# Optimization experiments

Hardware: AMD Instinct MI355X
Metric: run time of the kernel (lower is better)

Reference implementation:

```python
import jax, jax.numpy as jnp
import numpy as np

B, T, H, E = 4, 8192, 512, 2048  # batch, seq, hidden (num_dims), embed (num_embeds)
LN_EPS = 1e-5


def _layernorm(x, g, b):
    m = x.mean(-1, keepdims=True)
    v = ((x - m) ** 2).mean(-1, keepdims=True)
    return (x - m) * jax.lax.rsqrt(v + LN_EPS) * g + b


def setup_inputs() -> dict:
    key = jax.random.key(0)
    ks = jax.random.split(key, 8)
    C = 64
    tri = jnp.tril(jnp.ones((C, C), jnp.float32))
    kw = 1.0 / np.sqrt(C)
    inp = {
        "x": jax.random.normal(ks[0], (B, T, H), jnp.float32),
        "ln1_g": jnp.ones((H,), jnp.float32),
        "ln1_b": jnp.zeros((H,), jnp.float32),
        # TriLinear weights: (features, features), lower-triangular masked at init
        "W1": jax.random.uniform(ks[1], (C, C), jnp.float32, -kw, kw) * tri,
        "W2": jax.random.uniform(ks[2], (C, C), jnp.float32, -kw, kw) * tri,
        "ln2_g": jnp.ones((H,), jnp.float32),
        "ln2_b": jnp.zeros((H,), jnp.float32),
        # ffw: Linear(H->E), sin, Linear(E->H); stored (in, out)
        "fw1": jax.random.uniform(ks[3], (H, E), jnp.float32, -1.0 / np.sqrt(H), 1.0 / np.sqrt(H)),
        "fb1": jax.random.uniform(ks[4], (E,), jnp.float32, -1.0 / np.sqrt(H), 1.0 / np.sqrt(H)),
        "fw2": jax.random.uniform(ks[5], (E, H), jnp.float32, -1.0 / np.sqrt(E), 1.0 / np.sqrt(E)),
        "fb2": jax.random.uniform(ks[6], (H,), jnp.float32, -1.0 / np.sqrt(E), 1.0 / np.sqrt(E)),
        "chunk_size": 64,
        "stride": 32,
    }
    return inp


def reference(x, ln1_g, ln1_b, W1, W2, ln2_g, ln2_b, fw1, fb1, fw2, fb2, chunk_size, stride):
    Bb, Tt, Hh = x.shape
    C = chunk_size
    starts = jnp.arange(0, Tt, stride)              # (N,)
    pos = starts[:, None] + jnp.arange(C)           # (N, C)
    valid = (pos < Tt)
    vmask = valid[None, :, :, None].astype(x.dtype)
    safe = jnp.minimum(pos, Tt - 1)
    chunks = x[:, safe] * vmask                     # (B, N, C, H): padded chunks (zeros past T)
    resid = chunks
    cn = _layernorm(chunks, ln1_g, ln1_b)
    tri = jnp.tril(jnp.ones((C, C), x.dtype))
    # TriLinear on time axis (torch transposes to (B,H,C); einsum avoids the transpose)
    y = jnp.einsum('ts,bnsh->bnth', W1 * tri, cn)
    y = jnp.einsum('ts,bnsh->bnth', W2 * tri, y)
    c2 = y + resid
    h = _layernorm(c2, ln2_g, ln2_b)
    h = jnp.sin(h @ fw1 + fb1) @ fw2 + fb2
    out_chunks = (h + c2) * vmask                   # zero the padded tail (torch truncates it)
    flat = safe.reshape(-1)                         # (N*C,)
    out = jnp.zeros_like(x).at[:, flat].add(out_chunks.reshape(Bb, -1, Hh))
    counts = jnp.zeros((Tt,), x.dtype).at[flat].add(valid.reshape(-1).astype(x.dtype))
    return out / jnp.maximum(counts, 1.0)[None, :, None]
```

## Files before the change

### kernel.cpp

```cpp
#include <hip/hip_runtime.h>
#include <math.h>

#define TB 4
#define TT 8192
#define TH 512
#define TE 2048
#define NCHUNK 256
#define GCTOT 1024

typedef unsigned short u16;
typedef short bf8v __attribute__((ext_vector_type(8)));
typedef float f4v __attribute__((ext_vector_type(4)));

__device__ __forceinline__ float bu2f(u16 u) {
    unsigned int x = ((unsigned int)u) << 16; float f; __builtin_memcpy(&f, &x, 4); return f;
}
__device__ __forceinline__ u16 f2bu(float f) {
    unsigned int x; __builtin_memcpy(&x, &f, 4);
    x = x + 0x7fffu + ((x >> 16) & 1u);
    return (u16)(x >> 16);
}

__global__ __launch_bounds__(256) void make_Mt(const float* __restrict__ W1,
                                               const float* __restrict__ W2,
                                               float* __restrict__ Mt) {
    __shared__ float w1[64 * 64];
    __shared__ float w2[64 * 64];
    for (int i = threadIdx.x; i < 4096; i += 256) { w1[i] = W1[i]; w2[i] = W2[i]; }
    __syncthreads();
    for (int i = threadIdx.x; i < 4096; i += 256) {
        int t = i >> 6, s = i & 63;
        float a = 0.f;
        if (t >= s) for (int k = s; k <= t; ++k) a += w2[t * 64 + k] * w1[k * 64 + s];
        Mt[s * 64 + t] = a;
    }
}

__global__ __launch_bounds__(256) void transpose_b(const float* __restrict__ in,
                                                   u16* __restrict__ out, int R, int C) {
    __shared__ u16 tile[64][65];
    const int bx = blockIdx.x, by = blockIdx.y;
    const int tx = threadIdx.x & 63, ty = threadIdx.x >> 6;
#pragma unroll
    for (int i = 0; i < 16; ++i) {
        int r = ty + i * 4;
        tile[r][tx] = f2bu(in[(size_t)(by * 64 + r) * C + bx * 64 + tx]);
    }
    __syncthreads();
#pragma unroll
    for (int i = 0; i < 16; ++i) {
        int r = ty + i * 4;
        out[(size_t)(bx * 64 + r) * R + by * 64 + tx] = tile[tx][r];
    }
}

__global__ __launch_bounds__(256) void ln_stats(const float* __restrict__ x,
                                                float2* __restrict__ st) {
    const int wave = threadIdx.x >> 6, lane = threadIdx.x & 63;
    const size_t row = (size_t)blockIdx.x * 4 + wave;
    const float4* p = (const float4*)(x + row * TH);
    float4 a = p[lane * 2], b = p[lane * 2 + 1];
    float s = 0.f, q = 0.f;
    float v[8] = {a.x, a.y, a.z, a.w, b.x, b.y, b.z, b.w};
#pragma unroll
    for (int i = 0; i < 8; ++i) { s += v[i]; q += v[i] * v[i]; }
#pragma unroll
    for (int o = 32; o; o >>= 1) { s += __shfl_xor(s, o); q += __shfl_xor(q, o); }
    const float mean = s * (1.f / TH);
    float var = q * (1.f / TH) - mean * mean;
    if (var < 0.f) var = 0.f;
    if (lane == 0) st[row] = make_float2(mean, rsqrtf(var + 1e-5f));
}

__global__ __launch_bounds__(256) void ln_rows(const u16* __restrict__ in,
                                               u16* __restrict__ out,
                                               const float* __restrict__ g,
                                               const float* __restrict__ b) {
    const int wave = threadIdx.x >> 6, lane = threadIdx.x & 63;
    const size_t row = (size_t)blockIdx.x * 4 + wave;
    uint4 raw = *((const uint4*)(in + row * TH) + lane);
    const u16* e = (const u16*)&raw;
    float v[8]; float s = 0.f, q = 0.f;
#pragma unroll
    for (int i = 0; i < 8; ++i) { v[i] = bu2f(e[i]); s += v[i]; q += v[i] * v[i]; }
#pragma unroll
    for (int o = 32; o; o >>= 1) { s += __shfl_xor(s, o); q += __shfl_xor(q, o); }
    const float mean = s * (1.f / TH);
    float var = q * (1.f / TH) - mean * mean;
    if (var < 0.f) var = 0.f;
    const float rstd = rsqrtf(var + 1e-5f);
    float4 g0 = ((const float4*)g)[lane * 2], g1 = ((const float4*)g)[lane * 2 + 1];
    float4 b0 = ((const float4*)b)[lane * 2], b1 = ((const float4*)b)[lane * 2 + 1];
    float ge[8] = {g0.x, g0.y, g0.z, g0.w, g1.x, g1.y, g1.z, g1.w};
    float be[8] = {b0.x, b0.y, b0.z, b0.w, b1.x, b1.y, b1.z, b1.w};
    u16 ov[8];
#pragma unroll
    for (int i = 0; i < 8; ++i) ov[i] = f2bu((v[i] - mean) * rstd * ge[i] + be[i]);
    *((uint4*)(out + row * TH) + lane) = *(uint4*)ov;
}

__global__ __launch_bounds__(256) void trilinear_f(const float* __restrict__ x,
                                                   const float2* __restrict__ st,
                                                   const float* __restrict__ g,
                                                   const float* __restrict__ bb,
                                                   const float* __restrict__ Mt,
                                                   u16* __restrict__ c2s,
                                                   int gc0) {
    const int ln = blockIdx.x;
    const int gc = gc0 + ln;
    const int b = gc >> 8, n = gc & 255;
    const int h = (blockIdx.y << 8) + threadIdx.x;
    const int base = n * 32;
    const float gh = g[h], bh = bb[h];
    float acc[64];
#pragma unroll
    for (int t = 0; t < 64; ++t) acc[t] = 0.f;
    for (int s = 0; s < 64; ++s) {
        int pos = base + s; if (pos > TT - 1) pos = TT - 1;
        const size_t ro = (size_t)b * TT + pos;
        const float2 mr = st[ro];
        const float cn = (x[ro * TH + h] - mr.x) * mr.y * gh + bh;
        const float* m = Mt + s * 64;
#pragma unroll
        for (int t = 0; t < 64; ++t) acc[t] += m[t] * cn;
    }
#pragma unroll
    for (int t = 0; t < 64; ++t) {
        int pos = base + t; if (pos > TT - 1) pos = TT - 1;
        const float resid = x[((size_t)b * TT + pos) * TH + h];
        c2s[(size_t)(ln * 64 + t) * TH + h] = f2bu(acc[t] + resid);
    }
}

template <int MODE>
__global__ __launch_bounds__(512, 2) void gemm_p2(const u16* __restrict__ A,
                                                  const u16* __restrict__ Bt,
                                                  u16* __restrict__ C,
                                                  const float* __restrict__ bias,
                                                  const u16* __restrict__ addp,
                                                  int N, int K) {
    __shared__ __attribute__((aligned(16))) u16 lA[3][256 * 64];
    __shared__ __attribute__((aligned(16))) u16 lB[3][128 * 64];
    const int tid = threadIdx.x;
    const int wave = tid >> 6;
    const int lane = tid & 63;
    const int wr = wave >> 1;
    const int wc = wave & 1;
    const int fr = lane & 15;
    const int fq = (lane >> 4) << 3;
    const int s8 = (fr & 7) << 3;

    int bx = blockIdx.x, by = blockIdx.y;
    const int gx = gridDim.x;
    const int nwg = gx * (int)gridDim.y;
    if ((nwg & 7) == 0) {
        const int bid = by * gx + bx;
        const int swz = (bid & 7) * (nwg >> 3) + (bid >> 3);
        bx = swz % gx; by = swz / gx;
    }
    const int bm = by << 8;
    const int bn = bx << 7;

    const int srow = tid >> 3;
    const int gch = ((tid & 7) ^ (srow & 7)) << 3;
    const u16* pa = A + (size_t)(bm + srow) * K + gch;
    const u16* pb = Bt + (size_t)(bn + srow) * K + gch;
    const int ldsw = wave << 9;

    const int NT = K >> 6;
    f4v acc[4][4] = {};

    auto stage = [&](int t, int buf) {
        const size_t ko = (size_t)t << 6;
#pragma unroll
        for (int i = 0; i < 4; ++i)
            __builtin_amdgcn_global_load_lds(
                (const __attribute__((address_space(1))) void*)(pa + (size_t)(i * 64) * K + ko),
                (__attribute__((address_space(3))) void*)(&lA[buf][(i << 12) + ldsw]), 16, 0, 0);
#pragma unroll
        for (int i = 0; i < 2; ++i)
            __builtin_amdgcn_global_load_lds(
                (const __attribute__((address_space(1))) void*)(pb + (size_t)(i * 64) * K + ko),
                (__attribute__((address_space(3))) void*)(&lB[buf][(i << 12) + ldsw]), 16, 0, 0);
    };

    stage(0, 0);
    stage(1, 1);
    asm volatile("s_waitcnt vmcnt(6)" ::: "memory");
    asm volatile("s_barrier" ::: "memory");

    const int arow0 = (wr << 6) + fr;
    const int brow0 = (wc << 6) + fr;
    const int c0 = fq ^ s8;
    const int c1 = (32 + fq) ^ s8;

    int buf = 0;
    for (int t = 0; t < NT; ++t) {
        if (t + 2 < NT) {
            int sb = buf + 2; if (sb >= 3) sb -= 3;
            stage(t + 2, sb);
        }
        const u16* la = lA[buf];
        const u16* lb = lB[buf];
#pragma unroll
        for (int half = 0; half < 2; ++half) {
            const int cc = half ? c1 : c0;
            bf8v af[4], bf[4];
#pragma unroll
            for (int mi = 0; mi < 4; ++mi)
                af[mi] = *(const bf8v*)(la + ((arow0 + (mi << 4)) << 6) + cc);
#pragma unroll
            for (int ni = 0; ni < 4; ++ni)
                bf[ni] = *(const bf8v*)(lb + ((brow0 + (ni << 4)) << 6) + cc);
#pragma unroll
            for (int mi = 0; mi < 4; ++mi)
#pragma unroll
                for (int ni = 0; ni < 4; ++ni)
                    acc[mi][ni] = __builtin_amdgcn_mfma_f32_16x16x32_bf16(af[mi], bf[ni], acc[mi][ni], 0, 0, 0);
        }
        if (t + 1 < NT) {
            if (t + 2 < NT) asm volatile("s_waitcnt vmcnt(6)" ::: "memory");
            else            asm volatile("s_waitcnt vmcnt(0)" ::: "memory");
            asm volatile("s_barrier" ::: "memory");
        }
        buf = buf + 1; if (buf >= 3) buf -= 3;
    }

    const int rq = (lane >> 4) << 2;
#pragma unroll
    for (int mi = 0; mi < 4; ++mi) {
#pragma unroll
        for (int ni = 0; ni < 4; ++ni) {
            const int col = bn + (wc << 6) + (ni << 4) + fr;
            const float bv = bias[col];
#pragma unroll
            for (int r = 0; r < 4; ++r) {
                const int row = bm + (wr << 6) + (mi << 4) + rq + r;
                float v = acc[mi][ni][r] + bv;
                if (MODE == 1) v = __sinf(v);
                else v += bu2f(addp[(size_t)row * N + col]);
                C[(size_t)row * N + col] = f2bu(v);
            }
        }
    }
}

__global__ __launch_bounds__(256) void gather_slice(const u16* __restrict__ ocs,
                                                    const u16* __restrict__ carry,
                                                    float* __restrict__ out,
                                                    int gc0) {
    const int idx = blockIdx.x * 256 + threadIdx.x;
    const int h8 = idx & 63;
    const int prow = idx >> 6;
    const int ap = gc0 * 32 + prow;
    const int b = ap >> 13, t = ap & 8191;
    const int n = t >> 5, c = t & 31;
    const int ln = (b << 8) + n - gc0;
    uint4 r1 = *((const uint4*)ocs + (size_t)(ln * 64 + c) * 64 + h8);
    const u16* e1 = (const u16*)&r1;
    float ov[8];
    if (t < 32) {
#pragma unroll
        for (int i = 0; i < 8; ++i) ov[i] = bu2f(e1[i]);
    } else {
        uint4 r0;
        if (ln == 0) r0 = *((const uint4*)carry + (size_t)(c + 32) * 64 + h8);
        else         r0 = *((const uint4*)ocs + (size_t)((ln - 1) * 64 + c + 32) * 64 + h8);
        const u16* e0 = (const u16*)&r0;
#pragma unroll
        for (int i = 0; i < 8; ++i) ov[i] = 0.5f * (bu2f(e1[i]) + bu2f(e0[i]));
    }
    float4* dst = (float4*)(out + (size_t)ap * TH + h8 * 8);
    dst[0] = make_float4(ov[0], ov[1], ov[2], ov[3]);
    dst[1] = make_float4(ov[4], ov[5], ov[6], ov[7]);
}

__global__ __launch_bounds__(256) void save_carry(const u16* __restrict__ ocs,
                                                  u16* __restrict__ carry, int SC) {
    const int i = blockIdx.x * 256 + threadIdx.x;
    ((uint4*)carry)[i] = ((const uint4*)(ocs + (size_t)(SC - 1) * 64 * TH))[i];
}

extern "C" void kernel_launch(void* const* d_in, const int* in_sizes, int n_in,
                              void* d_out, int out_size, void* d_ws, size_t ws_size,
                              hipStream_t stream) {
    const float* x   = (const float*)d_in[0];
    const float* g1  = (const float*)d_in[1];
    const float* b1  = (const float*)d_in[2];
    const float* W1  = (const float*)d_in[3];
    const float* W2  = (const float*)d_in[4];
    const float* g2  = (const float*)d_in[5];
    const float* b2  = (const float*)d_in[6];
    const float* fw1 = (const float*)d_in[7];
    const float* fb1 = (const float*)d_in[8];
    const float* fw2 = (const float*)d_in[9];
    const float* fb2 = (const float*)d_in[10];
    float* out = (float*)d_out;
    char* ws = (char*)d_ws;

    size_t o = 0;
    auto take = [&](size_t n) { size_t r = o; o = (o + n + 255) & ~(size_t)255; return r; };
    float*  Mt    = (float*) (ws + take(64 * 64 * 4));
    u16*    f1t   = (u16*)   (ws + take((size_t)TE * TH * 2));
    u16*    f2t   = (u16*)   (ws + take((size_t)TH * TE * 2));
    float2* st1   = (float2*)(ws + take((size_t)TB * TT * 8));
    u16*    carry = (u16*)   (ws + take((size_t)64 * TH * 2));
    const size_t fixed = o;

    int SC = 4;
    for (int cand = 256; cand >= 4; cand >>= 1) {
        size_t per = (size_t)cand * 64 * (TH * 2 * 3 + TE * 2) + 4 * 256;
        if (fixed + per <= ws_size) { SC = cand; break; }
    }
    u16* c2s = (u16*)(ws + take((size_t)SC * 64 * TH * 2));
    u16* h2s = (u16*)(ws + take((size_t)SC * 64 * TH * 2));
    u16* ocs = (u16*)(ws + take((size_t)SC * 64 * TH * 2));
    u16* us  = (u16*)(ws + take((size_t)SC * 64 * TE * 2));
    const int SR = SC * 64;

    make_Mt<<<1, 256, 0, stream>>>(W1, W2, Mt);
    transpose_b<<<dim3(TE / 64, TH / 64), 256, 0, stream>>>(fw1, f1t, TH, TE);
    transpose_b<<<dim3(TH / 64, TE / 64), 256, 0, stream>>>(fw2, f2t, TE, TH);
    ln_stats<<<(TB * TT) / 4, 256, 0, stream>>>(x, st1);

    for (int gc0 = 0; gc0 < GCTOT; gc0 += SC) {
        trilinear_f<<<dim3(SC, TH / 256), 256, 0, stream>>>(x, st1, g1, b1, Mt, c2s, gc0);
        ln_rows<<<SR / 4, 256, 0, stream>>>(c2s, h2s, g2, b2);
        gemm_p2<1><<<dim3(TE / 128, SR / 256), 512, 0, stream>>>(
            h2s, f1t, us, fb1, (const u16*)nullptr, TE, TH);
        gemm_p2<2><<<dim3(TH / 128, SR / 256), 512, 0, stream>>>(
            us, f2t, ocs, fb2, c2s, TH, TE);
        gather_slice<<<SC * 8, 256, 0, stream>>>(ocs, carry, out, gc0);
        save_carry<<<16, 256, 0, stream>>>(ocs, carry, SC);
    }
}
```

Before: 779.4 us.

## Interleave GEMM prefetch, LDS reads and MFMA into four phased sub-steps

```diff
diff --git a/kernel.cpp b/kernel.cpp
--- a/kernel.cpp
+++ b/kernel.cpp
@@ -133,7 +133,7 @@
 }
 
 template <int MODE>
-__global__ __launch_bounds__(512, 2) void gemm_p2(const u16* __restrict__ A,
+__global__ __launch_bounds__(512, 2) void gemm_ph(const u16* __restrict__ A,
                                                   const u16* __restrict__ Bt,
                                                   u16* __restrict__ C,
                                                   const float* __restrict__ bias,
@@ -170,22 +170,21 @@
     const int NT = K >> 6;
     f4v acc[4][4] = {};
 
-    auto stage = [&](int t, int buf) {
-        const size_t ko = (size_t)t << 6;
-#pragma unroll
-        for (int i = 0; i < 4; ++i)
-            __builtin_amdgcn_global_load_lds(
-                (const __attribute__((address_space(1))) void*)(pa + (size_t)(i * 64) * K + ko),
-                (__attribute__((address_space(3))) void*)(&lA[buf][(i << 12) + ldsw]), 16, 0, 0);
-#pragma unroll
-        for (int i = 0; i < 2; ++i)
-            __builtin_amdgcn_global_load_lds(
-                (const __attribute__((address_space(1))) void*)(pb + (size_t)(i * 64) * K + ko),
-                (__attribute__((address_space(3))) void*)(&lB[buf][(i << 12) + ldsw]), 16, 0, 0);
+    auto stageA = [&](int t, int buf2, int i) {
+        __builtin_amdgcn_global_load_lds(
+            (const __attribute__((address_space(1))) void*)(pa + (size_t)(i * 64) * K + ((size_t)t << 6)),
+            (__attribute__((address_space(3))) void*)(&lA[buf2][(i << 12) + ldsw]), 16, 0, 0);
     };
-
-    stage(0, 0);
-    stage(1, 1);
+    auto stageB = [&](int t, int buf2, int i) {
+        __builtin_amdgcn_global_load_lds(
+            (const __attribute__((address_space(1))) void*)(pb + (size_t)(i * 64) * K + ((size_t)t << 6)),
+            (__attribute__((address_space(3))) void*)(&lB[buf2][(i << 12) + ldsw]), 16, 0, 0);
+    };
+
+    stageA(0, 0, 0); stageA(0, 0, 1); stageA(0, 0, 2); stageA(0, 0, 3);
+    stageB(0, 0, 0); stageB(0, 0, 1);
+    stageA(1, 1, 0); stageA(1, 1, 1); stageA(1, 1, 2); stageA(1, 1, 3);
+    stageB(1, 1, 0); stageB(1, 1, 1);
     asm volatile("s_waitcnt vmcnt(6)" ::: "memory");
     asm volatile("s_barrier" ::: "memory");
 
@@ -196,33 +195,86 @@
 
     int buf = 0;
     for (int t = 0; t < NT; ++t) {
-        if (t + 2 < NT) {
-            int sb = buf + 2; if (sb >= 3) sb -= 3;
-            stage(t + 2, sb);
-        }
         const u16* la = lA[buf];
         const u16* lb = lB[buf];
-#pragma unroll
-        for (int half = 0; half < 2; ++half) {
-            const int cc = half ? c1 : c0;
-            bf8v af[4], bf[4];
-#pragma unroll
-            for (int mi = 0; mi < 4; ++mi)
-                af[mi] = *(const bf8v*)(la + ((arow0 + (mi << 4)) << 6) + cc);
-#pragma unroll
-            for (int ni = 0; ni < 4; ++ni)
-                bf[ni] = *(const bf8v*)(lb + ((brow0 + (ni << 4)) << 6) + cc);
-#pragma unroll
-            for (int mi = 0; mi < 4; ++mi)
-#pragma unroll
-                for (int ni = 0; ni < 4; ++ni)
-                    acc[mi][ni] = __builtin_amdgcn_mfma_f32_16x16x32_bf16(af[mi], bf[ni], acc[mi][ni], 0, 0, 0);
+        int sb = buf + 2; if (sb >= 3) sb -= 3;
+        const bool pre = (t + 2 < NT);
+
+        bf8v bfr[4][2];
+        bf8v a0[2][2];
+        bf8v a1[2][2];
+
+        if (pre) { stageA(t + 2, sb, 0); stageA(t + 2, sb, 1); }
+#pragma unroll
+        for (int ni = 0; ni < 4; ++ni) {
+            bfr[ni][0] = *(const bf8v*)(lb + ((brow0 + (ni << 4)) << 6) + c0);
+            bfr[ni][1] = *(const bf8v*)(lb + ((brow0 + (ni << 4)) << 6) + c1);
         }
-        if (t + 1 < NT) {
-            if (t + 2 < NT) asm volatile("s_waitcnt vmcnt(6)" ::: "memory");
-            else            asm volatile("s_waitcnt vmcnt(0)" ::: "memory");
-            asm volatile("s_barrier" ::: "memory");
+#pragma unroll
+        for (int mi = 0; mi < 2; ++mi) {
+            a0[mi][0] = *(const bf8v*)(la + ((arow0 + (mi << 4)) << 6) + c0);
+            a0[mi][1] = *(const bf8v*)(la + ((arow0 + (mi << 4)) << 6) + c1);
         }
+        asm volatile("s_barrier" ::: "memory");
+        asm volatile("s_waitcnt lgkmcnt(0)" ::: "memory");
+        __builtin_amdgcn_s_setprio(1);
+#pragma unroll
+        for (int mi = 0; mi < 2; ++mi)
+#pragma unroll
+            for (int ni = 0; ni < 2; ++ni) {
+                acc[mi][ni] = __builtin_amdgcn_mfma_f32_16x16x32_bf16(a0[mi][0], bfr[ni][0], acc[mi][ni], 0, 0, 0);
+                acc[mi][ni] = __builtin_amdgcn_mfma_f32_16x16x32_bf16(a0[mi][1], bfr[ni][1], acc[mi][ni], 0, 0, 0);
+            }
+        __builtin_amdgcn_s_setprio(0);
+        asm volatile("s_barrier" ::: "memory");
+
+        if (pre) { stageA(t + 2, sb, 2); stageA(t + 2, sb, 3); }
+        asm volatile("s_barrier" ::: "memory");
+        __builtin_amdgcn_s_setprio(1);
+#pragma unroll
+        for (int mi = 0; mi < 2; ++mi)
+#pragma unroll
+            for (int ni = 0; ni < 2; ++ni) {
+                acc[mi][ni + 2] = __builtin_amdgcn_mfma_f32_16x16x32_bf16(a0[mi][0], bfr[ni + 2][0], acc[mi][ni + 2], 0, 0, 0);
+                acc[mi][ni + 2] = __builtin_amdgcn_mfma_f32_16x16x32_bf16(a0[mi][1], bfr[ni + 2][1], acc[mi][ni + 2], 0, 0, 0);
+            }
+        __builtin_amdgcn_s_setprio(0);
+        asm volatile("s_barrier" ::: "memory");
+
+        if (pre) stageB(t + 2, sb, 0);
+#pragma unroll
+        for (int mi = 0; mi < 2; ++mi) {
+            a1[mi][0] = *(const bf8v*)(la + ((arow0 + ((mi + 2) << 4)) << 6) + c0);
+            a1[mi][1] = *(const bf8v*)(la + ((arow0 + ((mi + 2) << 4)) << 6) + c1);
+        }
+        asm volatile("s_barrier" ::: "memory");
+        asm volatile("s_waitcnt lgkmcnt(0)" ::: "memory");
+        __builtin_amdgcn_s_setprio(1);
+#pragma unroll
+        for (int mi = 0; mi < 2; ++mi)
+#pragma unroll
+            for (int ni = 0; ni < 2; ++ni) {
+                acc[mi + 2][ni] = __builtin_amdgcn_mfma_f32_16x16x32_bf16(a1[mi][0], bfr[ni][0], acc[mi + 2][ni], 0, 0, 0);
+                acc[mi + 2][ni] = __builtin_amdgcn_mfma_f32_16x16x32_bf16(a1[mi][1], bfr[ni][1], acc[mi + 2][ni], 0, 0, 0);
+            }
+        __builtin_amdgcn_s_setprio(0);
+        asm volatile("s_barrier" ::: "memory");
+
+        if (pre) stageB(t + 2, sb, 1);
+        asm volatile("s_barrier" ::: "memory");
+        __builtin_amdgcn_s_setprio(1);
+#pragma unroll
+        for (int mi = 0; mi < 2; ++mi)
+#pragma unroll
+            for (int ni = 0; ni < 2; ++ni) {
+                acc[mi + 2][ni + 2] = __builtin_amdgcn_mfma_f32_16x16x32_bf16(a1[mi][0], bfr[ni + 2][0], acc[mi + 2][ni + 2], 0, 0, 0);
+                acc[mi + 2][ni + 2] = __builtin_amdgcn_mfma_f32_16x16x32_bf16(a1[mi][1], bfr[ni + 2][1], acc[mi + 2][ni + 2], 0, 0, 0);
+            }
+        __builtin_amdgcn_s_setprio(0);
+        if (pre)                asm volatile("s_waitcnt vmcnt(6)" ::: "memory");
+        else if (t + 1 < NT)    asm volatile("s_waitcnt vmcnt(0)" ::: "memory");
+        asm volatile("s_barrier" ::: "memory");
+
         buf = buf + 1; if (buf >= 3) buf -= 3;
     }
 
@@ -326,9 +378,9 @@
     for (int gc0 = 0; gc0 < GCTOT; gc0 += SC) {
         trilinear_f<<<dim3(SC, TH / 256), 256, 0, stream>>>(x, st1, g1, b1, Mt, c2s, gc0);
         ln_rows<<<SR / 4, 256, 0, stream>>>(c2s, h2s, g2, b2);
-        gemm_p2<1><<<dim3(TE / 128, SR / 256), 512, 0, stream>>>(
+        gemm_ph<1><<<dim3(TE / 128, SR / 256), 512, 0, stream>>>(
             h2s, f1t, us, fb1, (const u16*)nullptr, TE, TH);
-        gemm_p2<2><<<dim3(TH / 128, SR / 256), 512, 0, stream>>>(
+        gemm_ph<2><<<dim3(TH / 128, SR / 256), 512, 0, stream>>>(
             us, f2t, ocs, fb2, c2s, TH, TE);
         gather_slice<<<SC * 8, 256, 0, stream>>>(ocs, carry, out, gc0);
         save_carry<<<16, 256, 0, stream>>>(ocs, carry, SC);
```

New measurement: 866.2 us. 11.1% more time.

## Widen GEMM tile to 256x256 with double-buffered LDS and early-issued prefetch

Applied to the files above, without the earlier changes.

```diff
diff --git a/kernel.cpp b/kernel.cpp
--- a/kernel.cpp
+++ b/kernel.cpp
@@ -133,19 +133,19 @@
 }
 
 template <int MODE>
-__global__ __launch_bounds__(512, 2) void gemm_p2(const u16* __restrict__ A,
-                                                  const u16* __restrict__ Bt,
-                                                  u16* __restrict__ C,
-                                                  const float* __restrict__ bias,
-                                                  const u16* __restrict__ addp,
-                                                  int N, int K) {
-    __shared__ __attribute__((aligned(16))) u16 lA[3][256 * 64];
-    __shared__ __attribute__((aligned(16))) u16 lB[3][128 * 64];
+__global__ __launch_bounds__(512, 2) void gemm_w(const u16* __restrict__ A,
+                                                 const u16* __restrict__ Bt,
+                                                 u16* __restrict__ C,
+                                                 const float* __restrict__ bias,
+                                                 const u16* __restrict__ addp,
+                                                 int N, int K) {
+    __shared__ __attribute__((aligned(16))) u16 lA[2][256 * 64];
+    __shared__ __attribute__((aligned(16))) u16 lB[2][256 * 64];
     const int tid = threadIdx.x;
     const int wave = tid >> 6;
     const int lane = tid & 63;
-    const int wr = wave >> 1;
-    const int wc = wave & 1;
+    const int wr = wave >> 2;
+    const int wc = wave & 3;
     const int fr = lane & 15;
     const int fq = (lane >> 4) << 3;
     const int s8 = (fr & 7) << 3;
@@ -159,7 +159,7 @@
         bx = swz % gx; by = swz / gx;
     }
     const int bm = by << 8;
-    const int bn = bx << 7;
+    const int bn = bx << 8;
 
     const int srow = tid >> 3;
     const int gch = ((tid & 7) ^ (srow & 7)) << 3;
@@ -168,7 +168,7 @@
     const int ldsw = wave << 9;
 
     const int NT = K >> 6;
-    f4v acc[4][4] = {};
+    f4v acc[8][4] = {};
 
     auto stage = [&](int t, int buf) {
         const size_t ko = (size_t)t << 6;
@@ -178,7 +178,7 @@
                 (const __attribute__((address_space(1))) void*)(pa + (size_t)(i * 64) * K + ko),
                 (__attribute__((address_space(3))) void*)(&lA[buf][(i << 12) + ldsw]), 16, 0, 0);
 #pragma unroll
-        for (int i = 0; i < 2; ++i)
+        for (int i = 0; i < 4; ++i)
             __builtin_amdgcn_global_load_lds(
                 (const __attribute__((address_space(1))) void*)(pb + (size_t)(i * 64) * K + ko),
                 (__attribute__((address_space(3))) void*)(&lB[buf][(i << 12) + ldsw]), 16, 0, 0);
@@ -186,56 +186,59 @@
 
     stage(0, 0);
     stage(1, 1);
-    asm volatile("s_waitcnt vmcnt(6)" ::: "memory");
+    asm volatile("s_waitcnt vmcnt(8)" ::: "memory");
     asm volatile("s_barrier" ::: "memory");
 
-    const int arow0 = (wr << 6) + fr;
+    const int arow0 = (wr << 7) + fr;
     const int brow0 = (wc << 6) + fr;
     const int c0 = fq ^ s8;
     const int c1 = (32 + fq) ^ s8;
 
-    int buf = 0;
     for (int t = 0; t < NT; ++t) {
-        if (t + 2 < NT) {
-            int sb = buf + 2; if (sb >= 3) sb -= 3;
-            stage(t + 2, sb);
-        }
+        const int buf = t & 1;
         const u16* la = lA[buf];
         const u16* lb = lB[buf];
-#pragma unroll
-        for (int half = 0; half < 2; ++half) {
-            const int cc = half ? c1 : c0;
-            bf8v af[4], bf[4];
-#pragma unroll
-            for (int mi = 0; mi < 4; ++mi)
-                af[mi] = *(const bf8v*)(la + ((arow0 + (mi << 4)) << 6) + cc);
-#pragma unroll
-            for (int ni = 0; ni < 4; ++ni)
-                bf[ni] = *(const bf8v*)(lb + ((brow0 + (ni << 4)) << 6) + cc);
-#pragma unroll
-            for (int mi = 0; mi < 4; ++mi)
+        bf8v af[8][2], bf[4][2];
+#pragma unroll
+        for (int mi = 0; mi < 8; ++mi) {
+            af[mi][0] = *(const bf8v*)(la + ((arow0 + (mi << 4)) << 6) + c0);
+            af[mi][1] = *(const bf8v*)(la + ((arow0 + (mi << 4)) << 6) + c1);
+        }
+#pragma unroll
+        for (int ni = 0; ni < 4; ++ni) {
+            bf[ni][0] = *(const bf8v*)(lb + ((brow0 + (ni << 4)) << 6) + c0);
+            bf[ni][1] = *(const bf8v*)(lb + ((brow0 + (ni << 4)) << 6) + c1);
+        }
+        asm volatile("s_waitcnt lgkmcnt(0)" ::: "memory");
+        __builtin_amdgcn_sched_barrier(0);
+        asm volatile("s_barrier" ::: "memory");
+        if (t + 2 < NT) stage(t + 2, buf);
+        __builtin_amdgcn_s_setprio(1);
+#pragma unroll
+        for (int ks = 0; ks < 2; ++ks)
+#pragma unroll
+            for (int mi = 0; mi < 8; ++mi)
 #pragma unroll
                 for (int ni = 0; ni < 4; ++ni)
-                    acc[mi][ni] = __builtin_amdgcn_mfma_f32_16x16x32_bf16(af[mi], bf[ni], acc[mi][ni], 0, 0, 0);
-        }
+                    acc[mi][ni] = __builtin_amdgcn_mfma_f32_16x16x32_bf16(af[mi][ks], bf[ni][ks], acc[mi][ni], 0, 0, 0);
+        __builtin_amdgcn_s_setprio(0);
         if (t + 1 < NT) {
-            if (t + 2 < NT) asm volatile("s_waitcnt vmcnt(6)" ::: "memory");
+            if (t + 2 < NT) asm volatile("s_waitcnt vmcnt(8)" ::: "memory");
             else            asm volatile("s_waitcnt vmcnt(0)" ::: "memory");
             asm volatile("s_barrier" ::: "memory");
         }
-        buf = buf + 1; if (buf >= 3) buf -= 3;
     }
 
     const int rq = (lane >> 4) << 2;
 #pragma unroll
-    for (int mi = 0; mi < 4; ++mi) {
+    for (int mi = 0; mi < 8; ++mi) {
 #pragma unroll
         for (int ni = 0; ni < 4; ++ni) {
             const int col = bn + (wc << 6) + (ni << 4) + fr;
             const float bv = bias[col];
 #pragma unroll
             for (int r = 0; r < 4; ++r) {
-                const int row = bm + (wr << 6) + (mi << 4) + rq + r;
+                const int row = bm + (wr << 7) + (mi << 4) + rq + r;
                 float v = acc[mi][ni][r] + bv;
                 if (MODE == 1) v = __sinf(v);
                 else v += bu2f(addp[(size_t)row * N + col]);
@@ -326,9 +329,9 @@
     for (int gc0 = 0; gc0 < GCTOT; gc0 += SC) {
         trilinear_f<<<dim3(SC, TH / 256), 256, 0, stream>>>(x, st1, g1, b1, Mt, c2s, gc0);
         ln_rows<<<SR / 4, 256, 0, stream>>>(c2s, h2s, g2, b2);
-        gemm_p2<1><<<dim3(TE / 128, SR / 256), 512, 0, stream>>>(
+        gemm_w<1><<<dim3(TE / 256, SR / 256), 512, 0, stream>>>(
             h2s, f1t, us, fb1, (const u16*)nullptr, TE, TH);
-        gemm_p2<2><<<dim3(TH / 128, SR / 256), 512, 0, stream>>>(
+        gemm_w<2><<<dim3(TH / 256, SR / 256), 512, 0, stream>>>(
             us, f2t, ocs, fb2, c2s, TH, TE);
         gather_slice<<<SC * 8, 256, 0, stream>>>(ocs, carry, out, gc0);
         save_carry<<<16, 256, 0, stream>>>(ocs, carry, SC);
```

Result: no change. 790.1 us (+1.4%).
